# Kernel optimization log

Hardware: AMD Instinct MI355X
Metric: run time of the kernel (lower is better)

Reference implementation:

```python
import jax, jax.numpy as jnp
import numpy as np

XI = 4.0  # init kwarg


def _gaussian_kernel(xi: float):
    radius = int(3 * xi)
    coords = jnp.arange(-radius, radius + 1, dtype=jnp.float32)
    g1 = jnp.exp(-coords ** 2 / (2 * xi * xi))
    g1 = g1 / g1.sum()
    # dense 3D outer-product kernel, shape (K, K, K)
    g3 = g1[:, None, None] * g1[None, :, None] * g1[None, None, :]
    K = g3.shape[0]
    # grouped depthwise weight: (out=3, in/groups=1, K, K, K)
    return jnp.broadcast_to(g3[None, None], (3, 1, K, K, K))


def setup_inputs() -> dict:
    key = jax.random.key(0)
    x = jax.random.normal(key, (1, 3, 160, 160, 160), dtype=jnp.float32)
    kernel = _gaussian_kernel(XI)
    return {"x": x, "kernel": kernel}


def reference(x, kernel):
    # grouped Conv3d, groups=3 (depthwise), 'same' padding of radius each side
    r = (kernel.shape[-1] - 1) // 2
    return jax.lax.conv_general_dilated(
        x, kernel,
        window_strides=(1, 1, 1),
        padding=[(r, r), (r, r), (r, r)],
        dimension_numbers=("NCDHW", "OIDHW", "NCDHW"),
        feature_group_count=3,
    )
```

## Files before the change

### kernel.cpp

```cpp
#include <hip/hip_runtime.h>
#include <hip/hip_fp16.h>


#define NV 160
constexpr int KS    = 25;
constexpr int RAD   = 12;
constexpr int PLANE = NV * NV;
constexpr int VOL   = NV * NV * NV;
constexpr int TOT   = 3 * VOL;
constexpr int ROWS  = NV + 2 * RAD;

constexpr int PITCH = 17;
constexpr int OPT   = 10;
constexpr int WIN   = OPT + KS - 1;
constexpr int OROW  = 168;

constexpr int HC2   = 80;
constexpr int TR    = HC2 + 2 * RAD;
constexpr int TP2   = 84;
constexpr int NTASK = TR * 20;

__device__ __forceinline__ void pk(float2& a, float2 g, float2 v) {
    asm("v_pk_fma_f32 %0, %1, %2, %0" : "+v"(a) : "v"(g), "v"(v));
}

__device__ __forceinline__ void load_g(const float* __restrict__ k3, float* g) {
    float c   = k3[12 * 625 + 312];
    float g12 = cbrtf(c);
    float inv = 1.0f / (g12 * g12);
#pragma unroll
    for (int t = 0; t < KS; ++t) g[t] = k3[t * 625 + 312] * inv;
}

__global__ __launch_bounds__(256) void conv_w(const float* __restrict__ in,
                                              __half* __restrict__ out,
                                              const float* __restrict__ k3) {
    __shared__ float2 T[ROWS][PITCH];
    float gs[KS];
    load_g(k3, gs);
    float2 g2[KS];
#pragma unroll
    for (int t = 0; t < KS; ++t) g2[t] = make_float2(gs[t], gs[t]);

    int tid = threadIdx.x;
    int b   = blockIdx.x;
    int ht  = b % 5;
    int cd  = b / 5;
    int h0  = ht * 32;
    const float* base = in + (size_t)cd * PLANE;

    int wl = tid & 31, hq = tid >> 5;
#pragma unroll
    for (int hh = 0; hh < 2; ++hh) {
        int hp = hq + hh * 8;
        const float* r0 = base + (h0 + 2 * hp) * NV;
#pragma unroll
        for (int ib = 0; ib < ROWS; ib += 32) {
            int i = ib + wl;
            if (i < ROWS) {
                int wv = i - RAD;
                float a = 0.f, bb = 0.f;
                if (wv >= 0 && wv < NV) { a = r0[wv]; bb = r0[NV + wv]; }
                T[i][hp] = make_float2(a, bb);
            }
        }
    }
    __syncthreads();

    int p  = tid & 15;
    int ct = tid >> 4;
    int wb = ct * OPT;
    float2 acc[OPT];
#pragma unroll
    for (int j = 0; j < OPT; ++j) acc[j] = make_float2(0.f, 0.f);
#pragma unroll
    for (int it = 0; it < WIN; ++it) {
        float2 v = T[wb + it][p];
#pragma unroll
        for (int j = 0; j < OPT; ++j) {
            int t = it - j;
            if (t >= 0 && t < KS) pk(acc[j], g2[t], v);
        }
    }

    __syncthreads();
    __half* Ost = (__half*)(&T[0][0]);
#pragma unroll
    for (int j = 0; j < OPT; ++j) {
        Ost[(2 * p)     * OROW + wb + j] = __float2half_rn(acc[j].x);
        Ost[(2 * p + 1) * OROW + wb + j] = __float2half_rn(acc[j].y);
    }
    __syncthreads();
    __half* ob = out + (size_t)cd * PLANE + (size_t)h0 * NV;
#pragma unroll
    for (int it = 0; it < 3; ++it) {
        int task = it * 256 + tid;
        if (task < 640) {
            int chunk = task % 20, row = task / 20;
            uint4 v = *(const uint4*)(Ost + row * OROW + 8 * chunk);
            *(uint4*)(ob + (size_t)row * NV + 8 * chunk) = v;
        }
    }
}

__global__ __launch_bounds__(320) void conv_h(const __half* __restrict__ in,
                                              __half* __restrict__ out,
                                              const float* __restrict__ k3) {
    __shared__ __half2 T[TR][TP2];
    float gs[KS];
    load_g(k3, gs);
    float2 g2[KS];
#pragma unroll
    for (int t = 0; t < KS; ++t) g2[t] = make_float2(gs[t], gs[t]);

    int tid = threadIdx.x;
    int b   = blockIdx.x;
    int hh  = b & 1;
    int cd  = b >> 1;
    int h0  = hh * HC2;
    const __half* base = in + (size_t)cd * PLANE;

#pragma unroll
    for (int it = 0; it < 7; ++it) {
        int task = it * 320 + tid;
        if (task < NTASK) {
            int r = task / 20, k = task % 20;
            int hg = h0 - RAD + r;
            uint4 v = make_uint4(0u, 0u, 0u, 0u);
            if (hg >= 0 && hg < NV)
                v = *(const uint4*)(base + hg * NV + 8 * k);
            *(uint4*)(&T[r][4 * k]) = v;
        }
    }
    __syncthreads();

    int wp = tid % 80, oc = tid / 80;
#pragma unroll
    for (int hv = 0; hv < 2; ++hv) {
        int rb = (oc + 4 * hv) * OPT;
        float2 acc[OPT];
#pragma unroll
        for (int j = 0; j < OPT; ++j) acc[j] = make_float2(0.f, 0.f);
#pragma unroll
        for (int it = 0; it < WIN; ++it) {
            float2 v = __half22float2(T[rb + it][wp]);
#pragma unroll
            for (int j = 0; j < OPT; ++j) {
                int t = it - j;
                if (t >= 0 && t < KS) pk(acc[j], g2[t], v);
            }
        }
        __half* op = out + (size_t)cd * PLANE + (size_t)(h0 + rb) * NV + 2 * wp;
#pragma unroll
        for (int j = 0; j < OPT; ++j)
            *(__half2*)(op + j * NV) = __float22half2_rn(acc[j]);
    }
}

__global__ __launch_bounds__(320) void conv_d(const __half* __restrict__ in,
                                              float* __restrict__ out,
                                              const float* __restrict__ k3) {
    __shared__ __half2 T[TR][TP2];
    float gs[KS];
    load_g(k3, gs);
    float2 g2[KS];
#pragma unroll
    for (int t = 0; t < KS; ++t) g2[t] = make_float2(gs[t], gs[t]);

    int tid = threadIdx.x;
    int b   = blockIdx.x;
    int dh  = b & 1;
    int ch  = b >> 1;
    int c   = ch / NV, h = ch % NV;
    int d0  = dh * HC2;
    const __half* base = in + (size_t)c * VOL + h * NV;

#pragma unroll
    for (int it = 0; it < 7; ++it) {
        int task = it * 320 + tid;
        if (task < NTASK) {
            int r = task / 20, k = task % 20;
            int dg = d0 - RAD + r;
            uint4 v = make_uint4(0u, 0u, 0u, 0u);
            if (dg >= 0 && dg < NV)
                v = *(const uint4*)(base + (size_t)dg * PLANE + 8 * k);
            *(uint4*)(&T[r][4 * k]) = v;
        }
    }
    __syncthreads();

    int wp = tid % 80, oc = tid / 80;
#pragma unroll
    for (int hv = 0; hv < 2; ++hv) {
        int rb = (oc + 4 * hv) * OPT;
        float2 acc[OPT];
#pragma unroll
        for (int j = 0; j < OPT; ++j) acc[j] = make_float2(0.f, 0.f);
#pragma unroll
        for (int it = 0; it < WIN; ++it) {
            float2 v = __half22float2(T[rb + it][wp]);
#pragma unroll
            for (int j = 0; j < OPT; ++j) {
                int t = it - j;
                if (t >= 0 && t < KS) pk(acc[j], g2[t], v);
            }
        }
        float* op = out + (size_t)c * VOL + h * NV + 2 * wp;
#pragma unroll
        for (int j = 0; j < OPT; ++j)
            *(float2*)(op + (size_t)(d0 + rb + j) * PLANE) = acc[j];
    }
}

__global__ __launch_bounds__(256) void conv3d_direct(const float* __restrict__ x,
                                                     const float* __restrict__ k3,
                                                     float* __restrict__ out) {
    int idx = blockIdx.x * 256 + threadIdx.x;
    if (idx >= TOT) return;
    int w = idx % NV;
    int t = idx / NV;
    int h = t % NV; t /= NV;
    int d = t % NV;
    int c = t / NV;
    const float* kc = k3 + c * (KS * KS * KS);
    float acc = 0.f;
    for (int i = 0; i < KS; ++i) {
        int dd = d + i - RAD;
        if (dd < 0 || dd >= NV) continue;
        for (int j = 0; j < KS; ++j) {
            int hh = h + j - RAD;
            if (hh < 0 || hh >= NV) continue;
            const float* xr = x + (c * NV + dd) * NV * NV + hh * NV + (w - RAD);
            const float* kr = kc + (i * KS + j) * KS;
            int k0 = (RAD - w) > 0 ? (RAD - w) : 0;
            int k1 = (NV + RAD - w) < KS ? (NV + RAD - w) : KS;
            for (int k = k0; k < k1; ++k) acc += kr[k] * xr[k];
        }
    }
    out[idx] = acc;
}

extern "C" void kernel_launch(void* const* d_in, const int* in_sizes, int n_in,
                              void* d_out, int out_size, void* d_ws, size_t ws_size,
                              hipStream_t stream) {
    const float* x  = (const float*)d_in[0];
    const float* k3 = (const float*)d_in[1];
    float* out = (float*)d_out;

    if (ws_size >= (size_t)TOT * 2 * sizeof(__half)) {
        __half* tmpA = (__half*)d_ws;
        __half* tmpB = tmpA + TOT;
        conv_w<<<2400, 256, 0, stream>>>(x, tmpA, k3);
        conv_h<<<480 * 2, 320, 0, stream>>>(tmpA, tmpB, k3);
        conv_d<<<480 * 2, 320, 0, stream>>>(tmpB, out, k3);
    } else {
        conv3d_direct<<<(TOT + 255) / 256, 256, 0, stream>>>(x, k3, out);
    }
}
```

Measured before the change: 55.34 us.

## Restructure W-pass to row-major smem tile with float4 loads and direct stores

The W-direction pass now loads 16 full rows per block into a row-major shared tile with float4 global reads, instead of a transposed float2 tile built from scalar loads. Each thread convolves 10 consecutive outputs of one row with scalar FMAs and writes half2 directly to global, which removes the shared-memory staging and the two extra barriers on output. The cost is losing the packed FMA, so the arithmetic issue doubles. The odd pitch (189) may also cause bank conflicts, since threads in a row read at a stride of 10 floats.

```diff
diff --git a/kernel.cpp b/kernel.cpp
--- a/kernel.cpp
+++ b/kernel.cpp
@@ -8,12 +8,11 @@
 constexpr int PLANE = NV * NV;
 constexpr int VOL   = NV * NV * NV;
 constexpr int TOT   = 3 * VOL;
-constexpr int ROWS  = NV + 2 * RAD;
-
-constexpr int PITCH = 17;
+
+constexpr int WHR   = 16;
+constexpr int WPIT  = 189;
 constexpr int OPT   = 10;
 constexpr int WIN   = OPT + KS - 1;
-constexpr int OROW  = 168;
 
 constexpr int HC2   = 80;
 constexpr int TR    = HC2 + 2 * RAD;
@@ -35,72 +34,54 @@
 __global__ __launch_bounds__(256) void conv_w(const float* __restrict__ in,
                                               __half* __restrict__ out,
                                               const float* __restrict__ k3) {
-    __shared__ float2 T[ROWS][PITCH];
-    float gs[KS];
-    load_g(k3, gs);
-    float2 g2[KS];
-#pragma unroll
-    for (int t = 0; t < KS; ++t) g2[t] = make_float2(gs[t], gs[t]);
+    __shared__ float X[WHR][WPIT];
+    float g[KS];
+    load_g(k3, g);
 
     int tid = threadIdx.x;
     int b   = blockIdx.x;
-    int ht  = b % 5;
-    int cd  = b / 5;
-    int h0  = ht * 32;
-    const float* base = in + (size_t)cd * PLANE;
-
-    int wl = tid & 31, hq = tid >> 5;
-#pragma unroll
-    for (int hh = 0; hh < 2; ++hh) {
-        int hp = hq + hh * 8;
-        const float* r0 = base + (h0 + 2 * hp) * NV;
-#pragma unroll
-        for (int ib = 0; ib < ROWS; ib += 32) {
-            int i = ib + wl;
-            if (i < ROWS) {
-                int wv = i - RAD;
-                float a = 0.f, bb = 0.f;
-                if (wv >= 0 && wv < NV) { a = r0[wv]; bb = r0[NV + wv]; }
-                T[i][hp] = make_float2(a, bb);
-            }
+    int hc  = b % 10;
+    int cd  = b / 10;
+    int h0  = hc * WHR;
+    const float* base = in + (size_t)cd * PLANE + (size_t)h0 * NV;
+
+    for (int z = tid; z < WHR * 24; z += 256) {
+        int r = z / 24, u = z % 24;
+        X[r][u < 12 ? u : 160 + u] = 0.f;
+    }
+#pragma unroll
+    for (int it = 0; it < 3; ++it) {
+        int task = it * 256 + tid;
+        if (task < WHR * 40) {
+            int q = task % 40, r = task / 40;
+            float4 f = *(const float4*)(base + r * NV + 4 * q);
+            X[r][12 + 4 * q]     = f.x;
+            X[r][12 + 4 * q + 1] = f.y;
+            X[r][12 + 4 * q + 2] = f.z;
+            X[r][12 + 4 * q + 3] = f.w;
         }
     }
     __syncthreads();
 
-    int p  = tid & 15;
-    int ct = tid >> 4;
-    int wb = ct * OPT;
-    float2 acc[OPT];
-#pragma unroll
-    for (int j = 0; j < OPT; ++j) acc[j] = make_float2(0.f, 0.f);
+    int c = tid & 15;
+    int r = tid >> 4;
+    float acc[OPT];
+#pragma unroll
+    for (int j = 0; j < OPT; ++j) acc[j] = 0.f;
 #pragma unroll
     for (int it = 0; it < WIN; ++it) {
-        float2 v = T[wb + it][p];
+        float v = X[r][c * OPT + it];
 #pragma unroll
         for (int j = 0; j < OPT; ++j) {
             int t = it - j;
-            if (t >= 0 && t < KS) pk(acc[j], g2[t], v);
-        }
-    }
-
-    __syncthreads();
-    __half* Ost = (__half*)(&T[0][0]);
-#pragma unroll
-    for (int j = 0; j < OPT; ++j) {
-        Ost[(2 * p)     * OROW + wb + j] = __float2half_rn(acc[j].x);
-        Ost[(2 * p + 1) * OROW + wb + j] = __float2half_rn(acc[j].y);
-    }
-    __syncthreads();
-    __half* ob = out + (size_t)cd * PLANE + (size_t)h0 * NV;
-#pragma unroll
-    for (int it = 0; it < 3; ++it) {
-        int task = it * 256 + tid;
-        if (task < 640) {
-            int chunk = task % 20, row = task / 20;
-            uint4 v = *(const uint4*)(Ost + row * OROW + 8 * chunk);
-            *(uint4*)(ob + (size_t)row * NV + 8 * chunk) = v;
-        }
-    }
+            if (t >= 0 && t < KS) acc[j] = fmaf(g[t], v, acc[j]);
+        }
+    }
+    __half* ob = out + (size_t)cd * PLANE + (size_t)(h0 + r) * NV + c * OPT;
+#pragma unroll
+    for (int j = 0; j < OPT / 2; ++j)
+        *(__half2*)(ob + 2 * j) =
+            __float22half2_rn(make_float2(acc[2 * j], acc[2 * j + 1]));
 }
 
 __global__ __launch_bounds__(320) void conv_h(const __half* __restrict__ in,
@@ -250,7 +231,7 @@
     if (ws_size >= (size_t)TOT * 2 * sizeof(__half)) {
         __half* tmpA = (__half*)d_ws;
         __half* tmpB = tmpA + TOT;
-        conv_w<<<2400, 256, 0, stream>>>(x, tmpA, k3);
+        conv_w<<<480 * 10, 256, 0, stream>>>(x, tmpA, k3);
         conv_h<<<480 * 2, 320, 0, stream>>>(tmpA, tmpB, k3);
         conv_d<<<480 * 2, 320, 0, stream>>>(tmpB, out, k3);
     } else {
```

Result: no change. 56.35 us (+1.8%).

## Split halo tile load into two phases overlapping second-half loads with compute

Applied to the files above, without the earlier changes.

In conv_h and conv_d the shared tile is now loaded in two parts. The first 64 rows are stored to LDS and the block barriers, the remaining 40 rows are fetched into registers while the first output half (rows 0-39) is computed, and then those rows are written to LDS before a second barrier and the second half. The aim is to hide global load latency behind the first half's FMA work. In exchange it uses more registers per thread and adds a barrier, with manual waitcnt and sched_barrier handling.

```diff
diff --git a/kernel.cpp b/kernel.cpp
--- a/kernel.cpp
+++ b/kernel.cpp
@@ -18,7 +18,8 @@
 constexpr int HC2   = 80;
 constexpr int TR    = HC2 + 2 * RAD;
 constexpr int TP2   = 84;
-constexpr int NTASK = TR * 20;
+constexpr int ATASK = 64 * 20;
+constexpr int BTASK = 40 * 20;
 
 __device__ __forceinline__ void pk(float2& a, float2 g, float2 v) {
     asm("v_pk_fma_f32 %0, %1, %2, %0" : "+v"(a) : "v"(g), "v"(v));
@@ -120,24 +121,70 @@
     int h0  = hh * HC2;
     const __half* base = in + (size_t)cd * PLANE;
 
-#pragma unroll
-    for (int it = 0; it < 7; ++it) {
-        int task = it * 320 + tid;
-        if (task < NTASK) {
-            int r = task / 20, k = task % 20;
+    uint4 rA[4];
+#pragma unroll
+    for (int i = 0; i < 4; ++i) {
+        int task = i * 320 + tid;
+        int r = task / 20, k = task % 20;
+        int hg = h0 - RAD + r;
+        rA[i] = make_uint4(0u, 0u, 0u, 0u);
+        if (hg >= 0 && hg < NV) rA[i] = *(const uint4*)(base + hg * NV + 8 * k);
+    }
+#pragma unroll
+    for (int i = 0; i < 4; ++i) {
+        int task = i * 320 + tid;
+        int r = task / 20, k = task % 20;
+        *(uint4*)(&T[r][4 * k]) = rA[i];
+    }
+    uint4 rB[3];
+#pragma unroll
+    for (int i = 0; i < 3; ++i) {
+        int task = i * 320 + tid;
+        rB[i] = make_uint4(0u, 0u, 0u, 0u);
+        if (task < BTASK) {
+            int r = 64 + task / 20, k = task % 20;
             int hg = h0 - RAD + r;
-            uint4 v = make_uint4(0u, 0u, 0u, 0u);
-            if (hg >= 0 && hg < NV)
-                v = *(const uint4*)(base + hg * NV + 8 * k);
-            *(uint4*)(&T[r][4 * k]) = v;
-        }
-    }
-    __syncthreads();
+            if (hg >= 0 && hg < NV) rB[i] = *(const uint4*)(base + hg * NV + 8 * k);
+        }
+    }
+    asm volatile("s_waitcnt lgkmcnt(0)" ::: "memory");
+    __builtin_amdgcn_s_barrier();
+    __builtin_amdgcn_sched_barrier(0);
 
     int wp = tid % 80, oc = tid / 80;
-#pragma unroll
-    for (int hv = 0; hv < 2; ++hv) {
-        int rb = (oc + 4 * hv) * OPT;
+    {
+        int rb = oc * OPT;
+        float2 acc[OPT];
+#pragma unroll
+        for (int j = 0; j < OPT; ++j) acc[j] = make_float2(0.f, 0.f);
+#pragma unroll
+        for (int it = 0; it < WIN; ++it) {
+            float2 v = __half22float2(T[rb + it][wp]);
+#pragma unroll
+            for (int j = 0; j < OPT; ++j) {
+                int t = it - j;
+                if (t >= 0 && t < KS) pk(acc[j], g2[t], v);
+            }
+        }
+        __half* op = out + (size_t)cd * PLANE + (size_t)(h0 + rb) * NV + 2 * wp;
+#pragma unroll
+        for (int j = 0; j < OPT; ++j)
+            *(__half2*)(op + j * NV) = __float22half2_rn(acc[j]);
+    }
+    __builtin_amdgcn_sched_barrier(0);
+#pragma unroll
+    for (int i = 0; i < 3; ++i) {
+        int task = i * 320 + tid;
+        if (task < BTASK) {
+            int r = 64 + task / 20, k = task % 20;
+            *(uint4*)(&T[r][4 * k]) = rB[i];
+        }
+    }
+    asm volatile("s_waitcnt lgkmcnt(0)" ::: "memory");
+    __builtin_amdgcn_s_barrier();
+    __builtin_amdgcn_sched_barrier(0);
+    {
+        int rb = (oc + 4) * OPT;
         float2 acc[OPT];
 #pragma unroll
         for (int j = 0; j < OPT; ++j) acc[j] = make_float2(0.f, 0.f);
@@ -175,24 +222,72 @@
     int d0  = dh * HC2;
     const __half* base = in + (size_t)c * VOL + h * NV;
 
-#pragma unroll
-    for (int it = 0; it < 7; ++it) {
-        int task = it * 320 + tid;
-        if (task < NTASK) {
-            int r = task / 20, k = task % 20;
+    uint4 rA[4];
+#pragma unroll
+    for (int i = 0; i < 4; ++i) {
+        int task = i * 320 + tid;
+        int r = task / 20, k = task % 20;
+        int dg = d0 - RAD + r;
+        rA[i] = make_uint4(0u, 0u, 0u, 0u);
+        if (dg >= 0 && dg < NV)
+            rA[i] = *(const uint4*)(base + (size_t)dg * PLANE + 8 * k);
+    }
+#pragma unroll
+    for (int i = 0; i < 4; ++i) {
+        int task = i * 320 + tid;
+        int r = task / 20, k = task % 20;
+        *(uint4*)(&T[r][4 * k]) = rA[i];
+    }
+    uint4 rB[3];
+#pragma unroll
+    for (int i = 0; i < 3; ++i) {
+        int task = i * 320 + tid;
+        rB[i] = make_uint4(0u, 0u, 0u, 0u);
+        if (task < BTASK) {
+            int r = 64 + task / 20, k = task % 20;
             int dg = d0 - RAD + r;
-            uint4 v = make_uint4(0u, 0u, 0u, 0u);
             if (dg >= 0 && dg < NV)
-                v = *(const uint4*)(base + (size_t)dg * PLANE + 8 * k);
-            *(uint4*)(&T[r][4 * k]) = v;
-        }
-    }
-    __syncthreads();
+                rB[i] = *(const uint4*)(base + (size_t)dg * PLANE + 8 * k);
+        }
+    }
+    asm volatile("s_waitcnt lgkmcnt(0)" ::: "memory");
+    __builtin_amdgcn_s_barrier();
+    __builtin_amdgcn_sched_barrier(0);
 
     int wp = tid % 80, oc = tid / 80;
-#pragma unroll
-    for (int hv = 0; hv < 2; ++hv) {
-        int rb = (oc + 4 * hv) * OPT;
+    {
+        int rb = oc * OPT;
+        float2 acc[OPT];
+#pragma unroll
+        for (int j = 0; j < OPT; ++j) acc[j] = make_float2(0.f, 0.f);
+#pragma unroll
+        for (int it = 0; it < WIN; ++it) {
+            float2 v = __half22float2(T[rb + it][wp]);
+#pragma unroll
+            for (int j = 0; j < OPT; ++j) {
+                int t = it - j;
+                if (t >= 0 && t < KS) pk(acc[j], g2[t], v);
+            }
+        }
+        float* op = out + (size_t)c * VOL + h * NV + 2 * wp;
+#pragma unroll
+        for (int j = 0; j < OPT; ++j)
+            *(float2*)(op + (size_t)(d0 + rb + j) * PLANE) = acc[j];
+    }
+    __builtin_amdgcn_sched_barrier(0);
+#pragma unroll
+    for (int i = 0; i < 3; ++i) {
+        int task = i * 320 + tid;
+        if (task < BTASK) {
+            int r = 64 + task / 20, k = task % 20;
+            *(uint4*)(&T[r][4 * k]) = rB[i];
+        }
+    }
+    asm volatile("s_waitcnt lgkmcnt(0)" ::: "memory");
+    __builtin_amdgcn_s_barrier();
+    __builtin_amdgcn_sched_barrier(0);
+    {
+        int rb = (oc + 4) * OPT;
         float2 acc[OPT];
 #pragma unroll
         for (int j = 0; j < OPT; ++j) acc[j] = make_float2(0.f, 0.f);
```

Result: slower. 61.28 us (+10.7%).

## Keep Gaussian taps in SGPRs, exploit symmetry, double threads per block

Applied to the files above, without the earlier changes.

The 13 unique symmetric filter taps are loaded, made wave-uniform with readfirstlane, and passed as scalar-register operands to packed FMAs, which frees the 25 per-thread VGPR tap copies. Each thread now computes half as many outputs (5 in conv_w, one 10-row strip in conv_h/conv_d), so block sizes double to 512/640 threads with occupancy hints. Block indices in conv_w and conv_h are remapped to interleave planes across consecutive blocks. The intent is higher occupancy and lower register pressure, at the cost of less tap reuse per thread in conv_w and a risk that SGPR operand constraints or the 640-thread launch bound cause spills.

```diff
diff --git a/kernel.cpp b/kernel.cpp
--- a/kernel.cpp
+++ b/kernel.cpp
@@ -11,48 +11,58 @@
 constexpr int ROWS  = NV + 2 * RAD;
 
 constexpr int PITCH = 17;
-constexpr int OPT   = 10;
-constexpr int WIN   = OPT + KS - 1;
+constexpr int OPTW  = 5;
+constexpr int WINW  = OPTW + KS - 1;
 constexpr int OROW  = 168;
 
 constexpr int HC2   = 80;
 constexpr int TR    = HC2 + 2 * RAD;
 constexpr int TP2   = 84;
 constexpr int NTASK = TR * 20;
-
-__device__ __forceinline__ void pk(float2& a, float2 g, float2 v) {
-    asm("v_pk_fma_f32 %0, %1, %2, %0" : "+v"(a) : "v"(g), "v"(v));
-}
-
-__device__ __forceinline__ void load_g(const float* __restrict__ k3, float* g) {
+constexpr int OPT   = 10;
+constexpr int WIN   = OPT + KS - 1;
+
+#define GW2(t) g2[(t) < 13 ? (t) : 24 - (t)]
+
+__device__ __forceinline__ void pks(float2& a, float2 g, float2 v) {
+    asm("v_pk_fma_f32 %0, %1, %2, %0" : "+v"(a) : "s"(g), "v"(v));
+}
+
+__device__ __forceinline__ float uniformf(float x) {
+    return __int_as_float(__builtin_amdgcn_readfirstlane(__float_as_int(x)));
+}
+
+__device__ __forceinline__ void load_g13_sgpr(const float* __restrict__ k3,
+                                              float2* g2) {
     float c   = k3[12 * 625 + 312];
     float g12 = cbrtf(c);
     float inv = 1.0f / (g12 * g12);
 #pragma unroll
-    for (int t = 0; t < KS; ++t) g[t] = k3[t * 625 + 312] * inv;
-}
-
-__global__ __launch_bounds__(256) void conv_w(const float* __restrict__ in,
-                                              __half* __restrict__ out,
-                                              const float* __restrict__ k3) {
+    for (int t = 0; t < 13; ++t) {
+        float u = uniformf(k3[t * 625 + 312] * inv);
+        g2[t] = make_float2(u, u);
+    }
+}
+
+__global__ __launch_bounds__(512, 8) void conv_w(const float* __restrict__ in,
+                                                 __half* __restrict__ out,
+                                                 const float* __restrict__ k3) {
     __shared__ float2 T[ROWS][PITCH];
-    float gs[KS];
-    load_g(k3, gs);
-    float2 g2[KS];
-#pragma unroll
-    for (int t = 0; t < KS; ++t) g2[t] = make_float2(gs[t], gs[t]);
+    float2 g2[13];
+    load_g13_sgpr(k3, g2);
 
     int tid = threadIdx.x;
     int b   = blockIdx.x;
-    int ht  = b % 5;
-    int cd  = b / 5;
+    int x8  = b & 7;
+    int m   = b >> 3;
+    int q   = m / 5;
+    int ht  = m % 5;
+    int cd  = 8 * q + x8;
     int h0  = ht * 32;
     const float* base = in + (size_t)cd * PLANE;
 
-    int wl = tid & 31, hq = tid >> 5;
-#pragma unroll
-    for (int hh = 0; hh < 2; ++hh) {
-        int hp = hq + hh * 8;
+    int wl = tid & 31, hp = tid >> 5;
+    {
         const float* r0 = base + (h0 + 2 * hp) * NV;
 #pragma unroll
         for (int ib = 0; ib < ROWS; ib += 32) {
@@ -69,32 +79,32 @@
 
     int p  = tid & 15;
     int ct = tid >> 4;
-    int wb = ct * OPT;
-    float2 acc[OPT];
-#pragma unroll
-    for (int j = 0; j < OPT; ++j) acc[j] = make_float2(0.f, 0.f);
-#pragma unroll
-    for (int it = 0; it < WIN; ++it) {
+    int wb = ct * OPTW;
+    float2 acc[OPTW];
+#pragma unroll
+    for (int j = 0; j < OPTW; ++j) acc[j] = make_float2(0.f, 0.f);
+#pragma unroll
+    for (int it = 0; it < WINW; ++it) {
         float2 v = T[wb + it][p];
 #pragma unroll
-        for (int j = 0; j < OPT; ++j) {
+        for (int j = 0; j < OPTW; ++j) {
             int t = it - j;
-            if (t >= 0 && t < KS) pk(acc[j], g2[t], v);
+            if (t >= 0 && t < KS) pks(acc[j], GW2(t), v);
         }
     }
 
     __syncthreads();
     __half* Ost = (__half*)(&T[0][0]);
 #pragma unroll
-    for (int j = 0; j < OPT; ++j) {
+    for (int j = 0; j < OPTW; ++j) {
         Ost[(2 * p)     * OROW + wb + j] = __float2half_rn(acc[j].x);
         Ost[(2 * p + 1) * OROW + wb + j] = __float2half_rn(acc[j].y);
     }
     __syncthreads();
     __half* ob = out + (size_t)cd * PLANE + (size_t)h0 * NV;
 #pragma unroll
-    for (int it = 0; it < 3; ++it) {
-        int task = it * 256 + tid;
+    for (int it = 0; it < 2; ++it) {
+        int task = it * 512 + tid;
         if (task < 640) {
             int chunk = task % 20, row = task / 20;
             uint4 v = *(const uint4*)(Ost + row * OROW + 8 * chunk);
@@ -103,26 +113,26 @@
     }
 }
 
-__global__ __launch_bounds__(320) void conv_h(const __half* __restrict__ in,
-                                              __half* __restrict__ out,
-                                              const float* __restrict__ k3) {
+__global__ __launch_bounds__(640, 8) void conv_h(const __half* __restrict__ in,
+                                                 __half* __restrict__ out,
+                                                 const float* __restrict__ k3) {
     __shared__ __half2 T[TR][TP2];
-    float gs[KS];
-    load_g(k3, gs);
-    float2 g2[KS];
-#pragma unroll
-    for (int t = 0; t < KS; ++t) g2[t] = make_float2(gs[t], gs[t]);
+    float2 g2[13];
+    load_g13_sgpr(k3, g2);
 
     int tid = threadIdx.x;
     int b   = blockIdx.x;
-    int hh  = b & 1;
-    int cd  = b >> 1;
+    int x8  = b & 7;
+    int m   = b >> 3;
+    int q   = m >> 1;
+    int hh  = m & 1;
+    int cd  = 8 * q + x8;
     int h0  = hh * HC2;
     const __half* base = in + (size_t)cd * PLANE;
 
 #pragma unroll
-    for (int it = 0; it < 7; ++it) {
-        int task = it * 320 + tid;
+    for (int it = 0; it < 4; ++it) {
+        int task = it * 640 + tid;
         if (task < NTASK) {
             int r = task / 20, k = task % 20;
             int hg = h0 - RAD + r;
@@ -135,37 +145,31 @@
     __syncthreads();
 
     int wp = tid % 80, oc = tid / 80;
-#pragma unroll
-    for (int hv = 0; hv < 2; ++hv) {
-        int rb = (oc + 4 * hv) * OPT;
-        float2 acc[OPT];
-#pragma unroll
-        for (int j = 0; j < OPT; ++j) acc[j] = make_float2(0.f, 0.f);
-#pragma unroll
-        for (int it = 0; it < WIN; ++it) {
-            float2 v = __half22float2(T[rb + it][wp]);
-#pragma unroll
-            for (int j = 0; j < OPT; ++j) {
-                int t = it - j;
-                if (t >= 0 && t < KS) pk(acc[j], g2[t], v);
-            }
-        }
-        __half* op = out + (size_t)cd * PLANE + (size_t)(h0 + rb) * NV + 2 * wp;
-#pragma unroll
-        for (int j = 0; j < OPT; ++j)
-            *(__half2*)(op + j * NV) = __float22half2_rn(acc[j]);
-    }
-}
-
-__global__ __launch_bounds__(320) void conv_d(const __half* __restrict__ in,
-                                              float* __restrict__ out,
-                                              const float* __restrict__ k3) {
+    int rb = oc * OPT;
+    float2 acc[OPT];
+#pragma unroll
+    for (int j = 0; j < OPT; ++j) acc[j] = make_float2(0.f, 0.f);
+#pragma unroll
+    for (int it = 0; it < WIN; ++it) {
+        float2 v = __half22float2(T[rb + it][wp]);
+#pragma unroll
+        for (int j = 0; j < OPT; ++j) {
+            int t = it - j;
+            if (t >= 0 && t < KS) pks(acc[j], GW2(t), v);
+        }
+    }
+    __half* op = out + (size_t)cd * PLANE + (size_t)(h0 + rb) * NV + 2 * wp;
+#pragma unroll
+    for (int j = 0; j < OPT; ++j)
+        *(__half2*)(op + j * NV) = __float22half2_rn(acc[j]);
+}
+
+__global__ __launch_bounds__(640, 8) void conv_d(const __half* __restrict__ in,
+                                                 float* __restrict__ out,
+                                                 const float* __restrict__ k3) {
     __shared__ __half2 T[TR][TP2];
-    float gs[KS];
-    load_g(k3, gs);
-    float2 g2[KS];
-#pragma unroll
-    for (int t = 0; t < KS; ++t) g2[t] = make_float2(gs[t], gs[t]);
+    float2 g2[13];
+    load_g13_sgpr(k3, g2);
 
     int tid = threadIdx.x;
     int b   = blockIdx.x;
@@ -176,8 +180,8 @@
     const __half* base = in + (size_t)c * VOL + h * NV;
 
 #pragma unroll
-    for (int it = 0; it < 7; ++it) {
-        int task = it * 320 + tid;
+    for (int it = 0; it < 4; ++it) {
+        int task = it * 640 + tid;
         if (task < NTASK) {
             int r = task / 20, k = task % 20;
             int dg = d0 - RAD + r;
@@ -190,26 +194,23 @@
     __syncthreads();
 
     int wp = tid % 80, oc = tid / 80;
-#pragma unroll
-    for (int hv = 0; hv < 2; ++hv) {
-        int rb = (oc + 4 * hv) * OPT;
-        float2 acc[OPT];
-#pragma unroll
-        for (int j = 0; j < OPT; ++j) acc[j] = make_float2(0.f, 0.f);
-#pragma unroll
-        for (int it = 0; it < WIN; ++it) {
-            float2 v = __half22float2(T[rb + it][wp]);
-#pragma unroll
-            for (int j = 0; j < OPT; ++j) {
-                int t = it - j;
-                if (t >= 0 && t < KS) pk(acc[j], g2[t], v);
-            }
-        }
-        float* op = out + (size_t)c * VOL + h * NV + 2 * wp;
-#pragma unroll
-        for (int j = 0; j < OPT; ++j)
-            *(float2*)(op + (size_t)(d0 + rb + j) * PLANE) = acc[j];
-    }
+    int rb = oc * OPT;
+    float2 acc[OPT];
+#pragma unroll
+    for (int j = 0; j < OPT; ++j) acc[j] = make_float2(0.f, 0.f);
+#pragma unroll
+    for (int it = 0; it < WIN; ++it) {
+        float2 v = __half22float2(T[rb + it][wp]);
+#pragma unroll
+        for (int j = 0; j < OPT; ++j) {
+            int t = it - j;
+            if (t >= 0 && t < KS) pks(acc[j], GW2(t), v);
+        }
+    }
+    float* op = out + (size_t)c * VOL + h * NV + 2 * wp;
+#pragma unroll
+    for (int j = 0; j < OPT; ++j)
+        *(float2*)(op + (size_t)(d0 + rb + j) * PLANE) = acc[j];
 }
 
 __global__ __launch_bounds__(256) void conv3d_direct(const float* __restrict__ x,
@@ -250,9 +251,9 @@
     if (ws_size >= (size_t)TOT * 2 * sizeof(__half)) {
         __half* tmpA = (__half*)d_ws;
         __half* tmpB = tmpA + TOT;
-        conv_w<<<2400, 256, 0, stream>>>(x, tmpA, k3);
-        conv_h<<<480 * 2, 320, 0, stream>>>(tmpA, tmpB, k3);
-        conv_d<<<480 * 2, 320, 0, stream>>>(tmpB, out, k3);
+        conv_w<<<2400, 512, 0, stream>>>(x, tmpA, k3);
+        conv_h<<<960, 640, 0, stream>>>(tmpA, tmpB, k3);
+        conv_d<<<960, 640, 0, stream>>>(tmpB, out, k3);
     } else {
         conv3d_direct<<<(TOT + 255) / 256, 256, 0, stream>>>(x, k3, out);
     }
```

Result: no change. 56.17 us (+1.5%).
